# Kernel tuning notes

Hardware: AMD Instinct MI355X
Metric: run time of the kernel (lower is better)

## Reference

```python
import jax, jax.numpy as jnp
import numpy as np
import math

B, N, D, RANK = 16, 65536, 8, 2
IN_SIZE, OUT_SIZE = 4096, 4096
TWO_PI = 2.0 * math.pi


def setup_inputs() -> dict:
    key = jax.random.key(0)
    k = jax.random.split(key, 6)
    x = jax.random.normal(k[0], (B, IN_SIZE), jnp.float32)
    # means live in index space: dim0 in [0, OUT_SIZE), dim1 in [0, IN_SIZE)
    means = jax.random.uniform(k[1], (B, N, RANK), jnp.float32) * jnp.array(
        [OUT_SIZE - 1, IN_SIZE - 1], jnp.float32)
    sigmas = jax.random.uniform(k[2], (B, N), jnp.float32) * 2.0 + 0.5  # positive stddevs
    values = jax.random.normal(k[3], (B, N), jnp.float32)
    bias = jax.random.normal(k[4], (OUT_SIZE,), jnp.float32) * 0.1
    noise = jax.random.normal(k[5], (B, N, D, RANK), jnp.float32)  # reparam noise (torch.randn in sample())
    return {"x": x, "means": means, "sigmas": sigmas, "values": values,
            "bias": bias, "noise": noise}


def reference(x, means, sigmas, values, bias, noise):
    # --- sample(): d reparameterized MVN samples per (mean, sigma) -> [B,N,D,RANK]
    samples = noise * sigmas[:, :, None, None] + means[:, :, None, :]
    # --- densities(): isotropic Gaussian pdf of samples under their own MVN -> [B,N,D]
    diff = samples - means[:, :, None, :]
    products = jnp.sum(diff * diff, axis=-1)              # squared distances [B,N,D]
    s2 = (sigmas * sigmas)[:, :, None]                    # sigma^2, [B,N,1]
    den = jnp.sqrt((TWO_PI ** RANK) * s2 ** RANK)
    probs = jnp.exp(-products / (2.0 * s2)) / den         # [B,N,D]
    # normalize proportions over the D samples of each tuple
    probs = probs / jnp.sum(probs, axis=2, keepdims=True)
    # --- round and clamp to integer indices in w_shape = (OUT_SIZE, IN_SIZE)
    upper = jnp.array([OUT_SIZE - 1, IN_SIZE - 1], jnp.float32)
    ints = jnp.clip(jnp.round(samples), 0.0, upper).astype(jnp.int32)  # [B,N,D,2]
    # --- weighted values, flattened to N*D sparse entries per batch element
    vals = (values[:, :, None] * probs).reshape(B, N * D)
    out_idx = ints[..., 0].reshape(B, N * D)
    in_idx = ints[..., 1].reshape(B, N * D)
    # --- segmented sparse matvec: y[b, o] += vals * x[b, i]
    # (equivalent to the sorted grouped dot-product loop in the torch code)
    def one(xb, oi, ii, vb):
        return jnp.zeros((OUT_SIZE,), x.dtype).at[oi].add(vb * xb[ii])
    y = jax.vmap(one)(x, out_idx, in_idx, vals)           # [B, OUT_SIZE]
    return y + bias
```

## Files before the change

kernel.cpp:

```cpp
#include <hip/hip_runtime.h>
#include <math.h>

#define BB 16
#define NN 65536
#define DD 8
#define OUT_SIZE 4096
#define IN_SIZE 4096

#define BLOCKS_PER_B 32
#define NC (NN / BLOCKS_PER_B)
#define BLOCK_THREADS 1024

__global__ void init_out(const float* __restrict__ bias, float* __restrict__ y) {
    int i = blockIdx.x * blockDim.x + threadIdx.x;
    y[i] = bias[i & (OUT_SIZE - 1)];
}

__global__ __launch_bounds__(BLOCK_THREADS, 8)
void hyper_scatter(const float* __restrict__ x,
                   const float* __restrict__ means,
                   const float* __restrict__ sigmas,
                   const float* __restrict__ values,
                   const float* __restrict__ noise,
                   float* __restrict__ y) {
    __shared__ float ys[OUT_SIZE];

    const int b     = blockIdx.x / BLOCKS_PER_B;
    const int chunk = blockIdx.x % BLOCKS_PER_B;
    const int tid   = threadIdx.x;
    const float* xb = x + (size_t)b * IN_SIZE;

    {
        float4* ydst = (float4*)ys;
        if (tid < OUT_SIZE / 4) {
            ydst[tid] = make_float4(0.f, 0.f, 0.f, 0.f);
        }
    }
    __syncthreads();

    const int n0 = chunk * NC;
    #pragma unroll
    for (int nl = tid; nl < NC; nl += BLOCK_THREADS) {
        const size_t base = (size_t)b * NN + (size_t)(n0 + nl);
        const float2 mean  = ((const float2*)means)[base];
        const float  sigma = sigmas[base];
        const float  value = values[base];

        const float4* np4 = (const float4*)(noise + base * (size_t)(DD * 2));
        float4 nz0 = np4[0], nz1 = np4[1], nz2 = np4[2], nz3 = np4[3];
        float nr[DD * 2] = { nz0.x, nz0.y, nz0.z, nz0.w,
                             nz1.x, nz1.y, nz1.z, nz1.w,
                             nz2.x, nz2.y, nz2.z, nz2.w,
                             nz3.x, nz3.y, nz3.z, nz3.w };

        const float neg_inv_2s2 = -0.5f / (sigma * sigma);

        float p[DD];
        int   oi[DD], ii[DD];
        float psum = 0.f;
        #pragma unroll
        for (int d = 0; d < DD; ++d) {
            float s0 = __fadd_rn(__fmul_rn(nr[2 * d],     sigma), mean.x);
            float s1 = __fadd_rn(__fmul_rn(nr[2 * d + 1], sigma), mean.y);
            float d0 = s0 - mean.x;
            float d1 = s1 - mean.y;
            float q  = d0 * d0 + d1 * d1;
            float pd = __expf(q * neg_inv_2s2);
            p[d] = pd;
            psum += pd;
            oi[d] = (int)fminf(fmaxf(rintf(s0), 0.f), (float)(OUT_SIZE - 1));
            ii[d] = (int)fminf(fmaxf(rintf(s1), 0.f), (float)(IN_SIZE - 1));
        }

        float xv[DD];
        #pragma unroll
        for (int d = 0; d < DD; ++d) xv[d] = xb[ii[d]];

        const float wscale = value / psum;
        #pragma unroll
        for (int d = 0; d < DD; ++d) {
            atomicAdd(&ys[oi[d]], wscale * p[d] * xv[d]);
        }
    }
    __syncthreads();

    float* yb = y + (size_t)b * OUT_SIZE;
    #pragma unroll
    for (int o = tid; o < OUT_SIZE; o += BLOCK_THREADS) {
        unsafeAtomicAdd(&yb[o], ys[o]);
    }
}

extern "C" void kernel_launch(void* const* d_in, const int* in_sizes, int n_in,
                              void* d_out, int out_size, void* d_ws, size_t ws_size,
                              hipStream_t stream) {
    const float* x      = (const float*)d_in[0];
    const float* means  = (const float*)d_in[1];
    const float* sigmas = (const float*)d_in[2];
    const float* values = (const float*)d_in[3];
    const float* bias   = (const float*)d_in[4];
    const float* noise  = (const float*)d_in[5];
    float* y = (float*)d_out;

    init_out<<<(BB * OUT_SIZE) / 256, 256, 0, stream>>>(bias, y);
    hyper_scatter<<<BB * BLOCKS_PER_B, BLOCK_THREADS, 0, stream>>>(
        x, means, sigmas, values, noise, y);
}
```

Measured before the change: 144.1 us.

## Prefetch next tuple, stage x in LDS, and merge duplicate-output atomics

Halves blocks per batch so each thread handles four tuples, and software-pipelines the tuple loads by prefetching the next tuple into registers while the current one is computed. The x row is staged in shared memory, and gathers alternate between LDS and global to spread load across both paths. Samples within a tuple that land on the same output index are merged before the shared-memory atomic, so fewer atomics collide. The Gaussian is evaluated with exp2 and a hardware reciprocal. The costs are higher register pressure from the prefetched tuple and fewer, larger blocks.

```diff
diff --git a/kernel.cpp b/kernel.cpp
--- a/kernel.cpp
+++ b/kernel.cpp
@@ -7,16 +7,36 @@
 #define OUT_SIZE 4096
 #define IN_SIZE 4096
 
-#define BLOCKS_PER_B 32
+#define BLOCKS_PER_B 16
 #define NC (NN / BLOCKS_PER_B)
 #define BLOCK_THREADS 1024
+#define TPT (NC / BLOCK_THREADS)
 
 __global__ void init_out(const float* __restrict__ bias, float* __restrict__ y) {
     int i = blockIdx.x * blockDim.x + threadIdx.x;
     y[i] = bias[i & (OUT_SIZE - 1)];
 }
 
-__global__ __launch_bounds__(BLOCK_THREADS, 8)
+struct TupIn {
+    float4 nz[4];
+    float2 mean;
+    float  sigma, value;
+};
+
+__device__ __forceinline__ void load_tuple(TupIn& T,
+                                           const float* __restrict__ means,
+                                           const float* __restrict__ sigmas,
+                                           const float* __restrict__ values,
+                                           const float* __restrict__ noise,
+                                           size_t idx) {
+    T.mean  = ((const float2*)means)[idx];
+    T.sigma = sigmas[idx];
+    T.value = values[idx];
+    const float4* np4 = (const float4*)(noise + idx * (size_t)(DD * 2));
+    T.nz[0] = np4[0]; T.nz[1] = np4[1]; T.nz[2] = np4[2]; T.nz[3] = np4[3];
+}
+
+__global__ __launch_bounds__(BLOCK_THREADS, 4)
 void hyper_scatter(const float* __restrict__ x,
                    const float* __restrict__ means,
                    const float* __restrict__ sigmas,
@@ -24,63 +44,83 @@
                    const float* __restrict__ noise,
                    float* __restrict__ y) {
     __shared__ float ys[OUT_SIZE];
+    __shared__ float xs[IN_SIZE];
 
-    const int b     = blockIdx.x / BLOCKS_PER_B;
-    const int chunk = blockIdx.x % BLOCKS_PER_B;
+    const int b     = blockIdx.x >> 4;
+    const int chunk = blockIdx.x & (BLOCKS_PER_B - 1);
     const int tid   = threadIdx.x;
     const float* xb = x + (size_t)b * IN_SIZE;
 
-    {
-        float4* ydst = (float4*)ys;
-        if (tid < OUT_SIZE / 4) {
-            ydst[tid] = make_float4(0.f, 0.f, 0.f, 0.f);
-        }
-    }
+    ((float4*)ys)[tid] = make_float4(0.f, 0.f, 0.f, 0.f);
+    ((float4*)xs)[tid] = ((const float4*)xb)[tid];
     __syncthreads();
 
-    const int n0 = chunk * NC;
+    const size_t tb = (size_t)b * NN + (size_t)chunk * NC;
+
+    TupIn cur, nxt;
+    load_tuple(cur, means, sigmas, values, noise, tb + tid);
+
     #pragma unroll
-    for (int nl = tid; nl < NC; nl += BLOCK_THREADS) {
-        const size_t base = (size_t)b * NN + (size_t)(n0 + nl);
-        const float2 mean  = ((const float2*)means)[base];
-        const float  sigma = sigmas[base];
-        const float  value = values[base];
+    for (int t = 0; t < TPT; ++t) {
+        if (t + 1 < TPT)
+            load_tuple(nxt, means, sigmas, values, noise,
+                       tb + (size_t)(t + 1) * BLOCK_THREADS + tid);
 
-        const float4* np4 = (const float4*)(noise + base * (size_t)(DD * 2));
-        float4 nz0 = np4[0], nz1 = np4[1], nz2 = np4[2], nz3 = np4[3];
-        float nr[DD * 2] = { nz0.x, nz0.y, nz0.z, nz0.w,
-                             nz1.x, nz1.y, nz1.z, nz1.w,
-                             nz2.x, nz2.y, nz2.z, nz2.w,
-                             nz3.x, nz3.y, nz3.z, nz3.w };
+        const float nr[DD * 2] = {
+            cur.nz[0].x, cur.nz[0].y, cur.nz[0].z, cur.nz[0].w,
+            cur.nz[1].x, cur.nz[1].y, cur.nz[1].z, cur.nz[1].w,
+            cur.nz[2].x, cur.nz[2].y, cur.nz[2].z, cur.nz[2].w,
+            cur.nz[3].x, cur.nz[3].y, cur.nz[3].z, cur.nz[3].w };
 
-        const float neg_inv_2s2 = -0.5f / (sigma * sigma);
+        const float c2 = (-0.5f * 1.44269504088896f) / (cur.sigma * cur.sigma);
 
         float p[DD];
         int   oi[DD], ii[DD];
         float psum = 0.f;
         #pragma unroll
         for (int d = 0; d < DD; ++d) {
-            float s0 = __fadd_rn(__fmul_rn(nr[2 * d],     sigma), mean.x);
-            float s1 = __fadd_rn(__fmul_rn(nr[2 * d + 1], sigma), mean.y);
-            float d0 = s0 - mean.x;
-            float d1 = s1 - mean.y;
+            float s0 = __fadd_rn(__fmul_rn(nr[2 * d],     cur.sigma), cur.mean.x);
+            float s1 = __fadd_rn(__fmul_rn(nr[2 * d + 1], cur.sigma), cur.mean.y);
+            float d0 = s0 - cur.mean.x;
+            float d1 = s1 - cur.mean.y;
             float q  = d0 * d0 + d1 * d1;
-            float pd = __expf(q * neg_inv_2s2);
+            float pd = exp2f(q * c2);
             p[d] = pd;
             psum += pd;
             oi[d] = (int)fminf(fmaxf(rintf(s0), 0.f), (float)(OUT_SIZE - 1));
             ii[d] = (int)fminf(fmaxf(rintf(s1), 0.f), (float)(IN_SIZE - 1));
         }
+        const float wscale = cur.value * __builtin_amdgcn_rcpf(psum);
 
         float xv[DD];
         #pragma unroll
-        for (int d = 0; d < DD; ++d) xv[d] = xb[ii[d]];
+        for (int d = 0; d < DD; ++d)
+            xv[d] = (d & 1) ? xb[ii[d]] : xs[ii[d]];
 
-        const float wscale = value / psum;
+        float v[DD];
+        #pragma unroll
+        for (int d = 0; d < DD; ++d) v[d] = p[d] * xv[d];
+
+        bool dupO[DD];
+        dupO[0] = false;
+        #pragma unroll
+        for (int d = 1; d < DD; ++d) {
+            bool any = false;
+            #pragma unroll
+            for (int j = 0; j < d; ++j) {
+                bool m = (oi[j] == oi[d]);
+                if (m) v[j] += v[d];
+                any = any || m;
+            }
+            dupO[d] = any;
+        }
+
         #pragma unroll
         for (int d = 0; d < DD; ++d) {
-            atomicAdd(&ys[oi[d]], wscale * p[d] * xv[d]);
+            if (!dupO[d]) atomicAdd(&ys[oi[d]], wscale * v[d]);
         }
+
+        cur = nxt;
     }
     __syncthreads();
 
```

After: 129.3 us. 10.2% less time.
